# Performance work log

Hardware: AMD Instinct MI355X
Metric: run time of the kernel (lower is better)

Reference implementation:

```python
import jax, jax.numpy as jnp
import numpy as np

B, C, D, Q = 256, 1000, 128, 262144
PROTO_M = 0.99   # args.proto_m
TEMP = 0.01      # hardcoded temperature in forward


def setup_inputs() -> dict:
    key = jax.random.key(0)
    ks = jax.random.split(key, 8)
    return {
        'q': jax.random.normal(ks[0], (B, D), jnp.float32),
        'k': jax.random.normal(ks[1], (B, D), jnp.float32),
        'output': jax.random.normal(ks[2], (B, C), jnp.float32),
        'output2': jax.random.normal(ks[3], (B, C), jnp.float32),
        'partial_Y': (jax.random.uniform(ks[4], (B, C)) < 0.1).astype(jnp.float32),
        'prototypes': jax.random.normal(ks[5], (C, D), jnp.float32),
        'queue': jax.random.normal(ks[6], (Q, D), jnp.float32),
        'queue_pseudo': jax.random.uniform(ks[7], (Q,), dtype=jnp.float32),
    }


def reference(q, k, output, output2, partial_Y, prototypes, queue, queue_pseudo):
    # pseudo-label selection: softmax over (detached logits * candidate mask) / T
    predicted_scores = jax.nn.softmax(jax.lax.stop_gradient(output) * partial_Y / TEMP, axis=1)
    pseudo_labels_b = jnp.argmax(predicted_scores, axis=1)  # [B] int

    # prototype scores use prototypes BEFORE the EMA update (mm snapshots values)
    logits_prot = jnp.matmul(jax.lax.stop_gradient(q), prototypes.T)  # [B, C]
    score_prot = jax.nn.softmax(logits_prot, axis=1)

    # sequential per-sample EMA scatter into prototypes (order-dependent on dup labels)
    q_detached = jax.lax.stop_gradient(q)

    def ema_step(protos, xs):
        feat, lab = xs
        new_row = protos[lab] * PROTO_M + (1.0 - PROTO_M) * feat
        return protos.at[lab].set(new_row), None

    protos, _ = jax.lax.scan(ema_step, prototypes, (q_detached, pseudo_labels_b))
    # F.normalize(p=2, dim=1) with eps=1e-12 clamp
    protos = protos / jnp.maximum(jnp.linalg.norm(protos, axis=1, keepdims=True), 1e-12)

    features = jnp.concatenate([q, k, queue], axis=0)  # [2B+Q, D]
    pseudo_labels = jnp.concatenate([
        pseudo_labels_b.astype(jnp.float32),
        pseudo_labels_b.astype(jnp.float32),
        queue_pseudo,
    ], axis=0)  # [2B+Q]

    return (output, output2, features, pseudo_labels, score_prot, protos)
```

## Files before the change

kernel.cpp:

```cpp
#include <hip/hip_runtime.h>
#include <math.h>

#define B 256
#define C 1000
#define D 128
#define QN 262144

#define OFF_FEAT   512000
#define OFF_LBL    34131968
#define OFF_SCORE  34394624
#define OFF_PROTO  34650624

#define N_Q4   (QN * D / 4)
#define N_O4   (B * C / 4)
#define N_F4   (B * D / 4)
#define N_P4   (QN / 4)

#define DST_Q4   ((OFF_FEAT + 2 * B * D) / 4)
#define DST_O24  (B * C / 4)
#define DST_QF4  (OFF_FEAT / 4)
#define DST_KF4  (OFF_FEAT / 4 + N_F4)
#define DST_P4   ((OFF_LBL + 2 * B) / 4)

__global__ __launch_bounds__(256) void copyq_kernel(
    const float4* __restrict__ src, float4* __restrict__ dst)
{
    const size_t base = (size_t)blockIdx.x * 1024 + threadIdx.x;
    float4 a = src[base];
    float4 b = src[base + 256];
    float4 c = src[base + 512];
    float4 d = src[base + 768];
    dst[base]       = a;
    dst[base + 256] = b;
    dst[base + 512] = c;
    dst[base + 768] = d;
}

#define SM_O2  (N_O4)
#define SM_Q   (2 * N_O4)
#define SM_K   (2 * N_O4 + N_F4)
#define SM_P   (2 * N_O4 + 2 * N_F4)
#define SM_TOT (2 * N_O4 + 2 * N_F4 + N_P4)

__global__ __launch_bounds__(256) void copysmall_kernel(
    const float4* __restrict__ q,
    const float4* __restrict__ k,
    const float4* __restrict__ output,
    const float4* __restrict__ output2,
    const float4* __restrict__ queue_pseudo,
    float4* __restrict__ out4)
{
    size_t i = (size_t)blockIdx.x * blockDim.x + threadIdx.x;
    if (i >= SM_TOT) return;
    if (i < SM_O2)       out4[i]                    = output[i];
    else if (i < SM_Q)   out4[DST_O24 + (i - SM_O2)] = output2[i - SM_O2];
    else if (i < SM_K)   out4[DST_QF4 + (i - SM_Q)]  = q[i - SM_Q];
    else if (i < SM_P)   out4[DST_KF4 + (i - SM_K)]  = k[i - SM_K];
    else                 out4[DST_P4 + (i - SM_P)]   = queue_pseudo[i - SM_P];
}

__global__ __launch_bounds__(256) void argmax_kernel(
    const float* __restrict__ output,
    const float* __restrict__ partial_Y,
    int* __restrict__ labels,
    float* __restrict__ out_labels)
{
    const int b = blockIdx.x;
    const int tid = threadIdx.x;
    const float* row = output + (size_t)b * C;
    const float* msk = partial_Y + (size_t)b * C;

    float best = -INFINITY;
    int bidx = C;
    for (int c = tid; c < C; c += 256) {
        float v = row[c] * msk[c];
        if (v > best) { best = v; bidx = c; }
    }

    __shared__ float sv[256];
    __shared__ int   si[256];
    sv[tid] = best; si[tid] = bidx;
    __syncthreads();
    for (int s = 128; s > 0; s >>= 1) {
        if (tid < s) {
            float v2 = sv[tid + s]; int i2 = si[tid + s];
            if (v2 > sv[tid] || (v2 == sv[tid] && i2 < si[tid])) {
                sv[tid] = v2; si[tid] = i2;
            }
        }
        __syncthreads();
    }
    if (tid == 0) {
        int lab = si[0];
        labels[b] = lab;
        float f = (float)lab;
        out_labels[b]     = f;
        out_labels[B + b] = f;
    }
}

__global__ __launch_bounds__(256) void scoreprot_kernel(
    const float* __restrict__ q,
    const float* __restrict__ protos,
    float* __restrict__ out)
{
    const int b = blockIdx.x;
    const int tid = threadIdx.x;

    __shared__ float qs[D];
    if (tid < D) qs[tid] = q[(size_t)b * D + tid];
    __syncthreads();

    __shared__ float logits[C];
    for (int c = tid; c < C; c += 256) {
        const float4* p4 = (const float4*)(protos + (size_t)c * D);
        const float4* q4 = (const float4*)qs;
        float acc = 0.f;
        #pragma unroll
        for (int d = 0; d < D / 4; ++d) {
            float4 pv = p4[d];
            float4 qv = q4[d];
            acc += pv.x * qv.x + pv.y * qv.y + pv.z * qv.z + pv.w * qv.w;
        }
        logits[c] = acc;
    }
    __syncthreads();

    __shared__ float red[256];
    float lm = -INFINITY;
    for (int c = tid; c < C; c += 256) lm = fmaxf(lm, logits[c]);
    red[tid] = lm;
    __syncthreads();
    for (int s = 128; s > 0; s >>= 1) {
        if (tid < s) red[tid] = fmaxf(red[tid], red[tid + s]);
        __syncthreads();
    }
    const float m = red[0];
    __syncthreads();

    float psum = 0.f;
    for (int c = tid; c < C; c += 256) {
        float e = expf(logits[c] - m);
        logits[c] = e;
        psum += e;
    }
    red[tid] = psum;
    __syncthreads();
    for (int s = 128; s > 0; s >>= 1) {
        if (tid < s) red[tid] += red[tid + s];
        __syncthreads();
    }
    const float denom = red[0];

    for (int c = tid; c < C; c += 256)
        out[(size_t)b * C + c] = logits[c] / denom;
}

__global__ __launch_bounds__(128) void ema_kernel(
    const float* __restrict__ q,
    const float* __restrict__ protos_in,
    const int* __restrict__ labels,
    float* __restrict__ out)
{
    const int c = blockIdx.x;
    const int d = threadIdx.x;

    __shared__ int lab[B];
    for (int i = d; i < B; i += 128) lab[i] = labels[i];
    __syncthreads();

    float val = protos_in[(size_t)c * D + d];
    for (int b = 0; b < B; ++b) {
        if (lab[b] == c) {
            val = val * 0.99f + 0.01f * q[(size_t)b * D + d];
        }
    }

    __shared__ float ss[128];
    ss[d] = val * val;
    __syncthreads();
    for (int s = 64; s > 0; s >>= 1) {
        if (d < s) ss[d] += ss[d + s];
        __syncthreads();
    }
    float r = fmaxf(sqrtf(ss[0]), 1e-12f);
    out[(size_t)c * D + d] = val / r;
}

extern "C" void kernel_launch(void* const* d_in, const int* in_sizes, int n_in,
                              void* d_out, int out_size, void* d_ws, size_t ws_size,
                              hipStream_t stream) {
    const float* q            = (const float*)d_in[0];
    const float* k            = (const float*)d_in[1];
    const float* output       = (const float*)d_in[2];
    const float* output2      = (const float*)d_in[3];
    const float* partial_Y    = (const float*)d_in[4];
    const float* prototypes   = (const float*)d_in[5];
    const float* queue        = (const float*)d_in[6];
    const float* queue_pseudo = (const float*)d_in[7];

    float* out = (float*)d_out;
    int* labels = (int*)d_ws;

    argmax_kernel<<<B, 256, 0, stream>>>(output, partial_Y, labels, out + OFF_LBL);
    ema_kernel<<<C, 128, 0, stream>>>(q, prototypes, labels, out + OFF_PROTO);
    scoreprot_kernel<<<B, 256, 0, stream>>>(q, prototypes, out + OFF_SCORE);

    copyq_kernel<<<N_Q4 / 1024, 256, 0, stream>>>(
        (const float4*)queue, (float4*)out + DST_Q4);

    copysmall_kernel<<<(SM_TOT + 255) / 256, 256, 0, stream>>>(
        (const float4*)q, (const float4*)k,
        (const float4*)output, (const float4*)output2,
        (const float4*)queue_pseudo, (float4*)out);
}
```

Baseline: 294.5 us.

## Merge five launches into two heterogeneous kernels splitting queue copy

Replaces the five separate launches with two kernels whose blocks pick a role by block index. The first runs the argmax next to part of the queue copy. The second runs the EMA update (two prototypes per block), score softmax, the small copies and the rest of the queue copy. This is meant to cut launch overhead and let the bandwidth-bound queue copy overlap with the small compute stages. Only the argmax-to-EMA dependency is kept as a kernel boundary. The risk is load imbalance between block roles and more shared memory per block, since every role's arrays are allocated.

```diff
diff --git a/kernel.cpp b/kernel.cpp
--- a/kernel.cpp
+++ b/kernel.cpp
@@ -22,51 +22,46 @@
 #define DST_KF4  (OFF_FEAT / 4 + N_F4)
 #define DST_P4   ((OFF_LBL + 2 * B) / 4)
 
-__global__ __launch_bounds__(256) void copyq_kernel(
-    const float4* __restrict__ src, float4* __restrict__ dst)
-{
-    const size_t base = (size_t)blockIdx.x * 1024 + threadIdx.x;
-    float4 a = src[base];
-    float4 b = src[base + 256];
-    float4 c = src[base + 512];
-    float4 d = src[base + 768];
-    dst[base]       = a;
-    dst[base + 256] = b;
-    dst[base + 512] = c;
-    dst[base + 768] = d;
-}
-
 #define SM_O2  (N_O4)
 #define SM_Q   (2 * N_O4)
 #define SM_K   (2 * N_O4 + N_F4)
 #define SM_P   (2 * N_O4 + 2 * N_F4)
 #define SM_TOT (2 * N_O4 + 2 * N_F4 + N_P4)
 
-__global__ __launch_bounds__(256) void copysmall_kernel(
-    const float4* __restrict__ q,
-    const float4* __restrict__ k,
-    const float4* __restrict__ output,
-    const float4* __restrict__ output2,
-    const float4* __restrict__ queue_pseudo,
-    float4* __restrict__ out4)
-{
-    size_t i = (size_t)blockIdx.x * blockDim.x + threadIdx.x;
-    if (i >= SM_TOT) return;
-    if (i < SM_O2)       out4[i]                    = output[i];
-    else if (i < SM_Q)   out4[DST_O24 + (i - SM_O2)] = output2[i - SM_O2];
-    else if (i < SM_K)   out4[DST_QF4 + (i - SM_Q)]  = q[i - SM_Q];
-    else if (i < SM_P)   out4[DST_KF4 + (i - SM_K)]  = k[i - SM_K];
-    else                 out4[DST_P4 + (i - SM_P)]   = queue_pseudo[i - SM_P];
-}
-
-__global__ __launch_bounds__(256) void argmax_kernel(
+#define Q_TILES   (N_Q4 / 1024)
+#define K1_TILES  640
+#define K2_TILES  (Q_TILES - K1_TILES)
+
+#define R_EMA    500
+#define R_SCORE  (R_EMA + B)
+#define SM_BLKS  ((SM_TOT + 255) / 256)
+#define R_SMALL  (R_SCORE + SM_BLKS)
+#define K2_GRID  (R_SMALL + K2_TILES)
+
+__global__ __launch_bounds__(256) void k1_kernel(
     const float* __restrict__ output,
     const float* __restrict__ partial_Y,
+    const float4* __restrict__ queue,
     int* __restrict__ labels,
-    float* __restrict__ out_labels)
+    float* __restrict__ out)
 {
+    const int tid = threadIdx.x;
+
+    if (blockIdx.x >= B) {
+        const size_t base = (size_t)(blockIdx.x - B) * 1024 + tid;
+        float4* __restrict__ dst = (float4*)out + DST_Q4;
+        float4 a = queue[base];
+        float4 b = queue[base + 256];
+        float4 c = queue[base + 512];
+        float4 d = queue[base + 768];
+        dst[base]       = a;
+        dst[base + 256] = b;
+        dst[base + 512] = c;
+        dst[base + 768] = d;
+        return;
+    }
+
     const int b = blockIdx.x;
-    const int tid = threadIdx.x;
     const float* row = output + (size_t)b * C;
     const float* msk = partial_Y + (size_t)b * C;
 
@@ -94,97 +89,124 @@
         int lab = si[0];
         labels[b] = lab;
         float f = (float)lab;
-        out_labels[b]     = f;
-        out_labels[B + b] = f;
+        out[OFF_LBL + b]     = f;
+        out[OFF_LBL + B + b] = f;
     }
 }
 
-__global__ __launch_bounds__(256) void scoreprot_kernel(
+__global__ __launch_bounds__(256) void k2_kernel(
     const float* __restrict__ q,
-    const float* __restrict__ protos,
-    float* __restrict__ out)
-{
-    const int b = blockIdx.x;
-    const int tid = threadIdx.x;
-
-    __shared__ float qs[D];
-    if (tid < D) qs[tid] = q[(size_t)b * D + tid];
-    __syncthreads();
-
-    __shared__ float logits[C];
-    for (int c = tid; c < C; c += 256) {
-        const float4* p4 = (const float4*)(protos + (size_t)c * D);
-        const float4* q4 = (const float4*)qs;
-        float acc = 0.f;
-        #pragma unroll
-        for (int d = 0; d < D / 4; ++d) {
-            float4 pv = p4[d];
-            float4 qv = q4[d];
-            acc += pv.x * qv.x + pv.y * qv.y + pv.z * qv.z + pv.w * qv.w;
-        }
-        logits[c] = acc;
-    }
-    __syncthreads();
-
-    __shared__ float red[256];
-    float lm = -INFINITY;
-    for (int c = tid; c < C; c += 256) lm = fmaxf(lm, logits[c]);
-    red[tid] = lm;
-    __syncthreads();
-    for (int s = 128; s > 0; s >>= 1) {
-        if (tid < s) red[tid] = fmaxf(red[tid], red[tid + s]);
-        __syncthreads();
-    }
-    const float m = red[0];
-    __syncthreads();
-
-    float psum = 0.f;
-    for (int c = tid; c < C; c += 256) {
-        float e = expf(logits[c] - m);
-        logits[c] = e;
-        psum += e;
-    }
-    red[tid] = psum;
-    __syncthreads();
-    for (int s = 128; s > 0; s >>= 1) {
-        if (tid < s) red[tid] += red[tid + s];
-        __syncthreads();
-    }
-    const float denom = red[0];
-
-    for (int c = tid; c < C; c += 256)
-        out[(size_t)b * C + c] = logits[c] / denom;
-}
-
-__global__ __launch_bounds__(128) void ema_kernel(
-    const float* __restrict__ q,
-    const float* __restrict__ protos_in,
+    const float* __restrict__ kk,
+    const float* __restrict__ output,
+    const float* __restrict__ output2,
+    const float* __restrict__ prototypes,
+    const float4* __restrict__ queue,
+    const float* __restrict__ queue_pseudo,
     const int* __restrict__ labels,
     float* __restrict__ out)
 {
-    const int c = blockIdx.x;
-    const int d = threadIdx.x;
-
-    __shared__ int lab[B];
-    for (int i = d; i < B; i += 128) lab[i] = labels[i];
-    __syncthreads();
-
-    float val = protos_in[(size_t)c * D + d];
-    for (int b = 0; b < B; ++b) {
-        if (lab[b] == c) {
-            val = val * 0.99f + 0.01f * q[(size_t)b * D + d];
-        }
-    }
-
-    __shared__ float ss[128];
-    ss[d] = val * val;
-    __syncthreads();
-    for (int s = 64; s > 0; s >>= 1) {
-        if (d < s) ss[d] += ss[d + s];
-        __syncthreads();
-    }
-    float r = fmaxf(sqrtf(ss[0]), 1e-12f);
-    out[(size_t)c * D + d] = val / r;
+    const int bid = blockIdx.x;
+    const int tid = threadIdx.x;
+
+    if (bid < R_EMA) {
+        __shared__ int   lab[B];
+        __shared__ float ss[256];
+        const int c = 2 * bid + (tid >> 7);
+        const int d = tid & 127;
+        for (int i = tid; i < B; i += 256) lab[i] = labels[i];
+        __syncthreads();
+
+        float val = prototypes[(size_t)c * D + d];
+        for (int b = 0; b < B; ++b) {
+            if (lab[b] == c) {
+                val = val * 0.99f + 0.01f * q[(size_t)b * D + d];
+            }
+        }
+
+        ss[tid] = val * val;
+        __syncthreads();
+        for (int s = 64; s > 0; s >>= 1) {
+            if (d < s) ss[tid] += ss[tid + s];
+            __syncthreads();
+        }
+        float r = fmaxf(sqrtf(ss[tid & 128]), 1e-12f);
+        out[OFF_PROTO + (size_t)c * D + d] = val / r;
+        return;
+    }
+
+    if (bid < R_SCORE) {
+        const int b = bid - R_EMA;
+        __shared__ float qs[D];
+        __shared__ float logits[C];
+        __shared__ float red[256];
+        if (tid < D) qs[tid] = q[(size_t)b * D + tid];
+        __syncthreads();
+
+        for (int c = tid; c < C; c += 256) {
+            const float4* p4 = (const float4*)(prototypes + (size_t)c * D);
+            const float4* q4 = (const float4*)qs;
+            float acc = 0.f;
+            #pragma unroll
+            for (int d = 0; d < D / 4; ++d) {
+                float4 pv = p4[d];
+                float4 qv = q4[d];
+                acc += pv.x * qv.x + pv.y * qv.y + pv.z * qv.z + pv.w * qv.w;
+            }
+            logits[c] = acc;
+        }
+        __syncthreads();
+
+        float lm = -INFINITY;
+        for (int c = tid; c < C; c += 256) lm = fmaxf(lm, logits[c]);
+        red[tid] = lm;
+        __syncthreads();
+        for (int s = 128; s > 0; s >>= 1) {
+            if (tid < s) red[tid] = fmaxf(red[tid], red[tid + s]);
+            __syncthreads();
+        }
+        const float m = red[0];
+        __syncthreads();
+
+        float psum = 0.f;
+        for (int c = tid; c < C; c += 256) {
+            float e = expf(logits[c] - m);
+            logits[c] = e;
+            psum += e;
+        }
+        red[tid] = psum;
+        __syncthreads();
+        for (int s = 128; s > 0; s >>= 1) {
+            if (tid < s) red[tid] += red[tid + s];
+            __syncthreads();
+        }
+        const float denom = red[0];
+
+        for (int c = tid; c < C; c += 256)
+            out[OFF_SCORE + (size_t)b * C + c] = logits[c] / denom;
+        return;
+    }
+
+    if (bid < R_SMALL) {
+        const size_t i = (size_t)(bid - R_SCORE) * 256 + tid;
+        float4* __restrict__ out4 = (float4*)out;
+        if (i < SM_O2)       out4[i]                     = ((const float4*)output)[i];
+        else if (i < SM_Q)   out4[DST_O24 + (i - SM_O2)] = ((const float4*)output2)[i - SM_O2];
+        else if (i < SM_K)   out4[DST_QF4 + (i - SM_Q)]  = ((const float4*)q)[i - SM_Q];
+        else if (i < SM_P)   out4[DST_KF4 + (i - SM_K)]  = ((const float4*)kk)[i - SM_K];
+        else if (i < SM_TOT) out4[DST_P4 + (i - SM_P)]   = ((const float4*)queue_pseudo)[i - SM_P];
+        return;
+    }
+
+    const size_t base = ((size_t)(bid - R_SMALL) + K1_TILES) * 1024 + tid;
+    float4* __restrict__ dst = (float4*)out + DST_Q4;
+    float4 a = queue[base];
+    float4 b = queue[base + 256];
+    float4 c = queue[base + 512];
+    float4 d = queue[base + 768];
+    dst[base]       = a;
+    dst[base + 256] = b;
+    dst[base + 512] = c;
+    dst[base + 768] = d;
 }
 
 extern "C" void kernel_launch(void* const* d_in, const int* in_sizes, int n_in,
@@ -199,18 +221,13 @@
     const float* queue        = (const float*)d_in[6];
     const float* queue_pseudo = (const float*)d_in[7];
 
-    float* out = (float*)d_out;
+    float* out  = (float*)d_out;
     int* labels = (int*)d_ws;
 
-    argmax_kernel<<<B, 256, 0, stream>>>(output, partial_Y, labels, out + OFF_LBL);
-    ema_kernel<<<C, 128, 0, stream>>>(q, prototypes, labels, out + OFF_PROTO);
-    scoreprot_kernel<<<B, 256, 0, stream>>>(q, prototypes, out + OFF_SCORE);
-
-    copyq_kernel<<<N_Q4 / 1024, 256, 0, stream>>>(
-        (const float4*)queue, (float4*)out + DST_Q4);
-
-    copysmall_kernel<<<(SM_TOT + 255) / 256, 256, 0, stream>>>(
-        (const float4*)q, (const float4*)k,
-        (const float4*)output, (const float4*)output2,
-        (const float4*)queue_pseudo, (float4*)out);
+    k1_kernel<<<B + K1_TILES, 256, 0, stream>>>(
+        output, partial_Y, (const float4*)queue, labels, out);
+
+    k2_kernel<<<K2_GRID, 256, 0, stream>>>(
+        q, k, output, output2, prototypes,
+        (const float4*)queue, queue_pseudo, labels, out);
 }
```

New measurement: 271.7 us. 1.08x faster.
